# Kernel tuning notes

Hardware: AMD Instinct MI355X
Metric: run time of the kernel (lower is better)

## Reference

```python
import jax, jax.numpy as jnp
import numpy as np

B, E, K = 512, 4096, 1024      # batch, emb_dim, key_dim
M, L = 1024, 32                # mem_size, prompt_length
TOP_K = 4
EPS = 1e-12


def _l2norm(x, axis=-1):
    n = jnp.linalg.norm(x, axis=axis, keepdims=True)
    return x / jnp.maximum(n, EPS)


def setup_inputs() -> dict:
    key = jax.random.key(0)
    k1, k2, k3, k4 = jax.random.split(key, 4)
    return {
        "x_query": jax.random.normal(k1, (B, E), dtype=jnp.float32),
        "W_proj": jax.random.normal(k2, (K, E), dtype=jnp.float32) * 0.02,
        "prompt_memory": jax.random.normal(k3, (M, L, E), dtype=jnp.float32) * 0.02,
        "prompt_keys": jax.random.normal(k4, (M, K), dtype=jnp.float32) * 0.02,
        "top_k": TOP_K,
    }


def reference(x_query, W_proj, prompt_memory, prompt_keys, top_k):
    # x_proj = Linear(emb_dim -> key_dim, no bias): x @ W.T
    x_proj = jnp.einsum("be,ke->bk", x_query, W_proj)          # [B, K]
    x_norm = _l2norm(x_proj)                                     # [B, K]
    key_norm = _l2norm(prompt_keys)                              # [M, K]
    sim = jnp.einsum("bk,mk->bm", x_norm, key_norm)             # [B, M]
    _, idx = jax.lax.top_k(sim, top_k)                           # [B, top_k]
    sel_prompts = prompt_memory[idx]                             # [B, top_k, L, E]
    sel_keys = _l2norm(prompt_keys[idx], axis=2)                 # [B, top_k, K]
    refined = jnp.einsum("bk,btk->bt", x_norm, sel_keys)        # [B, top_k]
    w = jax.nn.softmax(refined, axis=1)                          # [B, top_k]
    # softmax-weighted sum over selected prompts
    out = jnp.einsum("btle,bt->ble", sel_prompts, w)            # [B, L, E]
    return out
```

## Files before the change

kernel.cpp:

```cpp
#include <hip/hip_runtime.h>
#include <math.h>

#define BDIM 512
#define EDIM 4096
#define KDIM 1024
#define MDIM 1024
#define LDIM 32
#define TOPK 4
#define EPSF 1e-12f

typedef __attribute__((ext_vector_type(8))) short short8;
typedef __attribute__((ext_vector_type(4))) float f32x4;

struct us4 { ushort x, y, z, w; };

__device__ inline ushort f2bf_rn(float x) {
    union { float f; unsigned u; } v; v.f = x;
    unsigned r = (v.u + 0x7FFF + ((v.u >> 16) & 1)) >> 16;
    return (ushort)r;
}
__device__ inline float bf2f(ushort h) {
    union { unsigned u; float f; } v; v.u = ((unsigned)h) << 16;
    return v.f;
}

__global__ __launch_bounds__(256)
void split_all_kernel(const float* __restrict__ xq, const float* __restrict__ wp,
                      const float* __restrict__ pk,
                      ushort* __restrict__ xq_h, ushort* __restrict__ xq_l,
                      ushort* __restrict__ wp_h, ushort* __restrict__ wp_l,
                      ushort* __restrict__ pk_h, ushort* __restrict__ pk_l,
                      float* __restrict__ kn)
{
    const int blk = blockIdx.x;
    const int t = threadIdx.x;
    const float* src; ushort* hi; ushort* lo; int base;
    bool do_norm = false; int rowbase = 0;
    if (blk < 512)       { src = xq; hi = xq_h; lo = xq_l; base = blk * 1024; }
    else if (blk < 1536) { src = wp; hi = wp_h; lo = wp_l; base = (blk - 512) * 1024; }
    else                 { src = pk; hi = pk_h; lo = pk_l; base = (blk - 1536) * 1024;
                           do_norm = true; rowbase = (blk - 1536) * 4; }

    __shared__ float wsum[4];
    const int lane = t & 63, wwid = t >> 6;

    #pragma unroll
    for (int it = 0; it < 4; ++it) {
        const int i = base + it * 256 + t;
        float4 v = ((const float4*)src)[i];
        us4 h, l;
        h.x = f2bf_rn(v.x); l.x = f2bf_rn(v.x - bf2f(h.x));
        h.y = f2bf_rn(v.y); l.y = f2bf_rn(v.y - bf2f(h.y));
        h.z = f2bf_rn(v.z); l.z = f2bf_rn(v.z - bf2f(h.z));
        h.w = f2bf_rn(v.w); l.w = f2bf_rn(v.w - bf2f(h.w));
        ((us4*)hi)[i] = h;
        ((us4*)lo)[i] = l;

        if (do_norm) {
            float sq = v.x * v.x + v.y * v.y + v.z * v.z + v.w * v.w;
            #pragma unroll
            for (int off = 32; off > 0; off >>= 1) sq += __shfl_down(sq, off, 64);
            __syncthreads();
            if (lane == 0) wsum[wwid] = sq;
            __syncthreads();
            if (t == 0)
                kn[rowbase + it] = sqrtf(wsum[0] + wsum[1] + wsum[2] + wsum[3]);
        }
    }
}

__global__ __launch_bounds__(256)
void gemm_mfma_split(const ushort* __restrict__ Ah, const ushort* __restrict__ Al,
                     const ushort* __restrict__ Bh, const ushort* __restrict__ Bl,
                     float* __restrict__ Cp, int M, int N, int K, int Kchunk)
{
    __shared__ ushort lds[4][64][40];

    const int t  = threadIdx.x;
    const int bn = blockIdx.x, bm = blockIdx.y, kz = blockIdx.z;

    const int srow = t >> 2, sg = t & 3;
    const size_t aoff = (size_t)(bm * 64 + srow) * K + sg * 8 + (size_t)kz * Kchunk;
    const size_t boff = (size_t)(bn * 64 + srow) * K + sg * 8 + (size_t)kz * Kchunk;

    const int lane = t & 63, wid = t >> 6;
    const int wr = wid >> 1, wc = wid & 1;
    const int fr = lane & 15, fg = lane >> 4;

    f32x4 acc[2][2];
    #pragma unroll
    for (int i = 0; i < 2; ++i)
        #pragma unroll
        for (int j = 0; j < 2; ++j)
            acc[i][j] = (f32x4){0.f, 0.f, 0.f, 0.f};

    short8 pA0 = *(const short8*)(Ah + aoff);
    short8 pA1 = *(const short8*)(Al + aoff);
    short8 pB0 = *(const short8*)(Bh + boff);
    short8 pB1 = *(const short8*)(Bl + boff);

    for (int k0 = 0; k0 < Kchunk; k0 += 32) {
        *(short8*)(&lds[0][srow][sg * 8]) = pA0;
        *(short8*)(&lds[1][srow][sg * 8]) = pA1;
        *(short8*)(&lds[2][srow][sg * 8]) = pB0;
        *(short8*)(&lds[3][srow][sg * 8]) = pB1;
        __syncthreads();

        if (k0 + 32 < Kchunk) {
            pA0 = *(const short8*)(Ah + aoff + k0 + 32);
            pA1 = *(const short8*)(Al + aoff + k0 + 32);
            pB0 = *(const short8*)(Bh + boff + k0 + 32);
            pB1 = *(const short8*)(Bl + boff + k0 + 32);
        }

        short8 ah[2], al[2], bh[2], bl[2];
        #pragma unroll
        for (int i = 0; i < 2; ++i) {
            ah[i] = *(const short8*)(&lds[0][wr * 32 + i * 16 + fr][fg * 8]);
            al[i] = *(const short8*)(&lds[1][wr * 32 + i * 16 + fr][fg * 8]);
            bh[i] = *(const short8*)(&lds[2][wc * 32 + i * 16 + fr][fg * 8]);
            bl[i] = *(const short8*)(&lds[3][wc * 32 + i * 16 + fr][fg * 8]);
        }
        #pragma unroll
        for (int i = 0; i < 2; ++i)
            #pragma unroll
            for (int j = 0; j < 2; ++j) {
                acc[i][j] = __builtin_amdgcn_mfma_f32_16x16x32_bf16(ah[i], bh[j], acc[i][j], 0, 0, 0);
                acc[i][j] = __builtin_amdgcn_mfma_f32_16x16x32_bf16(ah[i], bl[j], acc[i][j], 0, 0, 0);
                acc[i][j] = __builtin_amdgcn_mfma_f32_16x16x32_bf16(al[i], bh[j], acc[i][j], 0, 0, 0);
            }
        __syncthreads();
    }

    float* Cz = Cp + (size_t)kz * M * N;
    #pragma unroll
    for (int i = 0; i < 2; ++i)
        #pragma unroll
        for (int j = 0; j < 2; ++j)
            #pragma unroll
            for (int q = 0; q < 4; ++q) {
                int orow = bm * 64 + wr * 32 + i * 16 + (lane >> 4) * 4 + q;
                int ocol = bn * 64 + wc * 32 + j * 16 + (lane & 15);
                Cz[(size_t)orow * N + ocol] = acc[i][j][q];
            }
}

__global__ __launch_bounds__(256)
void reduce_split_norm_kernel(const float* __restrict__ Cp,
                              ushort* __restrict__ xh, ushort* __restrict__ xl,
                              float* __restrict__ xn)
{
    const int b = blockIdx.x;
    const int i = b * 256 + threadIdx.x;
    const int n4 = BDIM * KDIM / 4;

    float4 s = ((const float4*)Cp)[i];
    #pragma unroll
    for (int z = 1; z < 4; ++z) {
        float4 v = ((const float4*)Cp)[(size_t)z * n4 + i];
        s.x += v.x; s.y += v.y; s.z += v.z; s.w += v.w;
    }

    us4 h, l;
    h.x = f2bf_rn(s.x); l.x = f2bf_rn(s.x - bf2f(h.x));
    h.y = f2bf_rn(s.y); l.y = f2bf_rn(s.y - bf2f(h.y));
    h.z = f2bf_rn(s.z); l.z = f2bf_rn(s.z - bf2f(h.z));
    h.w = f2bf_rn(s.w); l.w = f2bf_rn(s.w - bf2f(h.w));
    ((us4*)xh)[i] = h;
    ((us4*)xl)[i] = l;

    float sq = s.x * s.x + s.y * s.y + s.z * s.z + s.w * s.w;
    #pragma unroll
    for (int off = 32; off > 0; off >>= 1) sq += __shfl_down(sq, off, 64);
    __shared__ float wsum[4];
    const int lane = threadIdx.x & 63, wwid = threadIdx.x >> 6;
    if (lane == 0) wsum[wwid] = sq;
    __syncthreads();
    if (threadIdx.x == 0)
        xn[b] = sqrtf(wsum[0] + wsum[1] + wsum[2] + wsum[3]);
}

__device__ inline bool tk_better(float x, int ix, float y, int iy) {
    return (x > y) || (x == y && ix < iy);
}
__device__ inline void tk_insert(float (&v)[4], int (&id)[4], float x, int m) {
    if (tk_better(x, m, v[3], id[3])) {
        v[3] = x; id[3] = m;
        if (tk_better(v[3], id[3], v[2], id[2])) {
            float tv = v[2]; int ti = id[2]; v[2] = v[3]; id[2] = id[3]; v[3] = tv; id[3] = ti;
            if (tk_better(v[2], id[2], v[1], id[1])) {
                tv = v[1]; ti = id[1]; v[1] = v[2]; id[1] = id[2]; v[2] = tv; id[2] = ti;
                if (tk_better(v[1], id[1], v[0], id[0])) {
                    tv = v[0]; ti = id[0]; v[0] = v[1]; id[0] = id[1]; v[1] = tv; id[1] = ti;
                }
            }
        }
    }
}
__global__ __launch_bounds__(64)
void topk_scale_kernel(const float* __restrict__ Cp2, const float* __restrict__ xn,
                       const float* __restrict__ kn,
                       int* __restrict__ topi, float* __restrict__ topv)
{
    const int b = blockIdx.x;
    const int lane = threadIdx.x;
    const float sb = 1.f / fmaxf(xn[b], EPSF);
    const float* r0 = Cp2 + (size_t)b * MDIM;
    const float* r1 = Cp2 + (size_t)BDIM * MDIM + (size_t)b * MDIM;

    float v[4] = {-INFINITY, -INFINITY, -INFINITY, -INFINITY};
    int id[4] = {-1, -1, -1, -1};
    for (int j = 0; j < MDIM / 64; ++j) {
        int m = j * 64 + lane;
        float s = (r0[m] + r1[m]) * sb / fmaxf(kn[m], EPSF);
        tk_insert(v, id, s, m);
    }
    for (int off = 32; off >= 1; off >>= 1) {
        float pv[4]; int pi[4];
        #pragma unroll
        for (int q = 0; q < 4; ++q) {
            pv[q] = __shfl_xor(v[q], off, 64);
            pi[q] = __shfl_xor(id[q], off, 64);
        }
        #pragma unroll
        for (int q = 0; q < 4; ++q) tk_insert(v, id, pv[q], pi[q]);
    }
    if (lane == 0) {
        #pragma unroll
        for (int q = 0; q < 4; ++q) { topv[b * 4 + q] = v[q]; topi[b * 4 + q] = id[q]; }
    }
}

__global__ __launch_bounds__(256)
void gather_out_kernel(const float* __restrict__ pm, const int* __restrict__ topi,
                       const float* __restrict__ topv, float* __restrict__ out)
{
    const int bl = blockIdx.x;
    const int b = bl & (BDIM - 1);
    const int l = bl >> 9;

    const int j0 = topi[b * 4 + 0], j1 = topi[b * 4 + 1], j2 = topi[b * 4 + 2], j3 = topi[b * 4 + 3];
    const float r0 = topv[b * 4 + 0], r1 = topv[b * 4 + 1], r2 = topv[b * 4 + 2], r3 = topv[b * 4 + 3];
    const float mx = fmaxf(fmaxf(r0, r1), fmaxf(r2, r3));
    const float e0 = expf(r0 - mx), e1 = expf(r1 - mx), e2 = expf(r2 - mx), e3 = expf(r3 - mx);
    const float inv = 1.f / (e0 + e1 + e2 + e3);
    const float w0 = e0 * inv, w1 = e1 * inv, w2 = e2 * inv, w3 = e3 * inv;

    const f32x4* p0 = (const f32x4*)(pm + ((size_t)j0 * LDIM + l) * EDIM);
    const f32x4* p1 = (const f32x4*)(pm + ((size_t)j1 * LDIM + l) * EDIM);
    const f32x4* p2 = (const f32x4*)(pm + ((size_t)j2 * LDIM + l) * EDIM);
    const f32x4* p3 = (const f32x4*)(pm + ((size_t)j3 * LDIM + l) * EDIM);
    f32x4* o = (f32x4*)(out + ((size_t)b * LDIM + l) * EDIM);

    for (int c = threadIdx.x; c < EDIM / 4; c += 256) {
        f32x4 a = p0[c], bb = p1[c], cc = p2[c], dd = p3[c];
        f32x4 r = w0 * a + w1 * bb + w2 * cc + w3 * dd;
        __builtin_nontemporal_store(r, &o[c]);
    }
}

extern "C" void kernel_launch(void* const* d_in, const int* in_sizes, int n_in,
                              void* d_out, int out_size, void* d_ws, size_t ws_size,
                              hipStream_t stream)
{
    const float* x_query = (const float*)d_in[0];
    const float* W_proj  = (const float*)d_in[1];
    const float* pm      = (const float*)d_in[2];
    const float* pkeys   = (const float*)d_in[3];
    float* out = (float*)d_out;

    char* w = (char*)d_ws;
    ushort* xq_h = (ushort*)w; w += (size_t)BDIM * EDIM * 2;
    ushort* xq_l = (ushort*)w; w += (size_t)BDIM * EDIM * 2;
    ushort* wp_h = (ushort*)w; w += (size_t)KDIM * EDIM * 2;
    ushort* wp_l = (ushort*)w; w += (size_t)KDIM * EDIM * 2;
    ushort* pk_h = (ushort*)w; w += (size_t)MDIM * KDIM * 2;
    ushort* pk_l = (ushort*)w; w += (size_t)MDIM * KDIM * 2;
    ushort* xp_h = (ushort*)w; w += (size_t)BDIM * KDIM * 2;
    ushort* xp_l = (ushort*)w; w += (size_t)BDIM * KDIM * 2;
    float* Cp1    = (float*)w; w += (size_t)4 * BDIM * KDIM * 4;
    float* Cp2    = (float*)w; w += (size_t)2 * BDIM * MDIM * 4;
    float* xn     = (float*)w; w += BDIM * 4;
    float* kn     = (float*)w; w += MDIM * 4;
    float* topv   = (float*)w; w += BDIM * TOPK * 4;
    int*   topi   = (int*)w;   w += BDIM * TOPK * 4;

    split_all_kernel<<<1792, 256, 0, stream>>>(
        x_query, W_proj, pkeys, xq_h, xq_l, wp_h, wp_l, pk_h, pk_l, kn);

    gemm_mfma_split<<<dim3(KDIM / 64, BDIM / 64, 4), 256, 0, stream>>>(
        xq_h, xq_l, wp_h, wp_l, Cp1, BDIM, KDIM, EDIM, EDIM / 4);

    reduce_split_norm_kernel<<<BDIM, 256, 0, stream>>>(Cp1, xp_h, xp_l, xn);

    gemm_mfma_split<<<dim3(MDIM / 64, BDIM / 64, 2), 256, 0, stream>>>(
        xp_h, xp_l, pk_h, pk_l, Cp2, BDIM, MDIM, KDIM, KDIM / 2);

    topk_scale_kernel<<<BDIM, 64, 0, stream>>>(Cp2, xn, kn, topi, topv);

    gather_out_kernel<<<BDIM * LDIM, 256, 0, stream>>>(pm, topi, topv, out);
}
```

Measured before the change: 240.3 us.

## Fuse bf16 hi/lo splitting into GEMM tile loads and drop split kernels

The separate split kernel and reduce-split kernel go away. Each GEMM now loads fp32 operands directly and splits them into bf16 hi/lo pairs while staging tiles into LDS. The second GEMM also sums the four split-K partials of the projection on the fly, and norm computation moves into a small combined kernel. The softmax weights are computed once per row in the top-k kernel instead of once per gather block. This removes kernel launches and the write and reread of the bf16 workspaces. In exchange the GEMM inner loops do more conversion arithmetic, read twice as many bytes per tile, and gemm2 reads four partial buffers redundantly across column blocks.

After: 248.4 us. +3.4%, slower.

```diff
diff --git a/kernel.cpp b/kernel.cpp
--- a/kernel.cpp
+++ b/kernel.cpp
@@ -12,8 +12,6 @@
 typedef __attribute__((ext_vector_type(8))) short short8;
 typedef __attribute__((ext_vector_type(4))) float f32x4;
 
-struct us4 { ushort x, y, z, w; };
-
 __device__ inline ushort f2bf_rn(float x) {
     union { float f; unsigned u; } v; v.f = x;
     unsigned r = (v.u + 0x7FFF + ((v.u >> 16) & 1)) >> 16;
@@ -23,65 +21,31 @@
     union { unsigned u; float f; } v; v.u = ((unsigned)h) << 16;
     return v.f;
 }
+__device__ inline void split8(const float4& v0, const float4& v1,
+                              short8& h, short8& l)
+{
+    float f[8] = {v0.x, v0.y, v0.z, v0.w, v1.x, v1.y, v1.z, v1.w};
+    #pragma unroll
+    for (int e = 0; e < 8; ++e) {
+        ushort hh = f2bf_rn(f[e]);
+        h[e] = (short)hh;
+        l[e] = (short)f2bf_rn(f[e] - bf2f(hh));
+    }
+}
 
 __global__ __launch_bounds__(256)
-void split_all_kernel(const float* __restrict__ xq, const float* __restrict__ wp,
-                      const float* __restrict__ pk,
-                      ushort* __restrict__ xq_h, ushort* __restrict__ xq_l,
-                      ushort* __restrict__ wp_h, ushort* __restrict__ wp_l,
-                      ushort* __restrict__ pk_h, ushort* __restrict__ pk_l,
-                      float* __restrict__ kn)
-{
-    const int blk = blockIdx.x;
-    const int t = threadIdx.x;
-    const float* src; ushort* hi; ushort* lo; int base;
-    bool do_norm = false; int rowbase = 0;
-    if (blk < 512)       { src = xq; hi = xq_h; lo = xq_l; base = blk * 1024; }
-    else if (blk < 1536) { src = wp; hi = wp_h; lo = wp_l; base = (blk - 512) * 1024; }
-    else                 { src = pk; hi = pk_h; lo = pk_l; base = (blk - 1536) * 1024;
-                           do_norm = true; rowbase = (blk - 1536) * 4; }
-
-    __shared__ float wsum[4];
-    const int lane = t & 63, wwid = t >> 6;
-
-    #pragma unroll
-    for (int it = 0; it < 4; ++it) {
-        const int i = base + it * 256 + t;
-        float4 v = ((const float4*)src)[i];
-        us4 h, l;
-        h.x = f2bf_rn(v.x); l.x = f2bf_rn(v.x - bf2f(h.x));
-        h.y = f2bf_rn(v.y); l.y = f2bf_rn(v.y - bf2f(h.y));
-        h.z = f2bf_rn(v.z); l.z = f2bf_rn(v.z - bf2f(h.z));
-        h.w = f2bf_rn(v.w); l.w = f2bf_rn(v.w - bf2f(h.w));
-        ((us4*)hi)[i] = h;
-        ((us4*)lo)[i] = l;
-
-        if (do_norm) {
-            float sq = v.x * v.x + v.y * v.y + v.z * v.z + v.w * v.w;
-            #pragma unroll
-            for (int off = 32; off > 0; off >>= 1) sq += __shfl_down(sq, off, 64);
-            __syncthreads();
-            if (lane == 0) wsum[wwid] = sq;
-            __syncthreads();
-            if (t == 0)
-                kn[rowbase + it] = sqrtf(wsum[0] + wsum[1] + wsum[2] + wsum[3]);
-        }
-    }
-}
-
-__global__ __launch_bounds__(256)
-void gemm_mfma_split(const ushort* __restrict__ Ah, const ushort* __restrict__ Al,
-                     const ushort* __restrict__ Bh, const ushort* __restrict__ Bl,
-                     float* __restrict__ Cp, int M, int N, int K, int Kchunk)
+void gemm1_kernel(const float* __restrict__ A, const float* __restrict__ B,
+                  float* __restrict__ Cp)
 {
     __shared__ ushort lds[4][64][40];
 
     const int t  = threadIdx.x;
     const int bn = blockIdx.x, bm = blockIdx.y, kz = blockIdx.z;
-
     const int srow = t >> 2, sg = t & 3;
-    const size_t aoff = (size_t)(bm * 64 + srow) * K + sg * 8 + (size_t)kz * Kchunk;
-    const size_t boff = (size_t)(bn * 64 + srow) * K + sg * 8 + (size_t)kz * Kchunk;
+    const int Kc = EDIM / 4;
+
+    const float* Ap = A + (size_t)(bm * 64 + srow) * EDIM + kz * Kc + sg * 8;
+    const float* Bp = B + (size_t)(bn * 64 + srow) * EDIM + kz * Kc + sg * 8;
 
     const int lane = t & 63, wid = t >> 6;
     const int wr = wid >> 1, wc = wid & 1;
@@ -94,23 +58,22 @@
         for (int j = 0; j < 2; ++j)
             acc[i][j] = (f32x4){0.f, 0.f, 0.f, 0.f};
 
-    short8 pA0 = *(const short8*)(Ah + aoff);
-    short8 pA1 = *(const short8*)(Al + aoff);
-    short8 pB0 = *(const short8*)(Bh + boff);
-    short8 pB1 = *(const short8*)(Bl + boff);
-
-    for (int k0 = 0; k0 < Kchunk; k0 += 32) {
-        *(short8*)(&lds[0][srow][sg * 8]) = pA0;
-        *(short8*)(&lds[1][srow][sg * 8]) = pA1;
-        *(short8*)(&lds[2][srow][sg * 8]) = pB0;
-        *(short8*)(&lds[3][srow][sg * 8]) = pB1;
+    float4 a0 = *(const float4*)(Ap),     a1 = *(const float4*)(Ap + 4);
+    float4 b0 = *(const float4*)(Bp),     b1 = *(const float4*)(Bp + 4);
+
+    for (int k0 = 0; k0 < Kc; k0 += 32) {
+        short8 ahs, als, bhs, bls;
+        split8(a0, a1, ahs, als);
+        split8(b0, b1, bhs, bls);
+        *(short8*)(&lds[0][srow][sg * 8]) = ahs;
+        *(short8*)(&lds[1][srow][sg * 8]) = als;
+        *(short8*)(&lds[2][srow][sg * 8]) = bhs;
+        *(short8*)(&lds[3][srow][sg * 8]) = bls;
         __syncthreads();
 
-        if (k0 + 32 < Kchunk) {
-            pA0 = *(const short8*)(Ah + aoff + k0 + 32);
-            pA1 = *(const short8*)(Al + aoff + k0 + 32);
-            pB0 = *(const short8*)(Bh + boff + k0 + 32);
-            pB1 = *(const short8*)(Bl + boff + k0 + 32);
+        if (k0 + 32 < Kc) {
+            a0 = *(const float4*)(Ap + k0 + 32); a1 = *(const float4*)(Ap + k0 + 36);
+            b0 = *(const float4*)(Bp + k0 + 32); b1 = *(const float4*)(Bp + k0 + 36);
         }
 
         short8 ah[2], al[2], bh[2], bl[2];
@@ -132,7 +95,7 @@
         __syncthreads();
     }
 
-    float* Cz = Cp + (size_t)kz * M * N;
+    float* Cz = Cp + (size_t)kz * BDIM * KDIM;
     #pragma unroll
     for (int i = 0; i < 2; ++i)
         #pragma unroll
@@ -141,43 +104,134 @@
             for (int q = 0; q < 4; ++q) {
                 int orow = bm * 64 + wr * 32 + i * 16 + (lane >> 4) * 4 + q;
                 int ocol = bn * 64 + wc * 32 + j * 16 + (lane & 15);
-                Cz[(size_t)orow * N + ocol] = acc[i][j][q];
+                Cz[(size_t)orow * KDIM + ocol] = acc[i][j][q];
             }
 }
 
 __global__ __launch_bounds__(256)
-void reduce_split_norm_kernel(const float* __restrict__ Cp,
-                              ushort* __restrict__ xh, ushort* __restrict__ xl,
-                              float* __restrict__ xn)
-{
-    const int b = blockIdx.x;
-    const int i = b * 256 + threadIdx.x;
-    const int n4 = BDIM * KDIM / 4;
-
-    float4 s = ((const float4*)Cp)[i];
-    #pragma unroll
-    for (int z = 1; z < 4; ++z) {
-        float4 v = ((const float4*)Cp)[(size_t)z * n4 + i];
-        s.x += v.x; s.y += v.y; s.z += v.z; s.w += v.w;
-    }
-
-    us4 h, l;
-    h.x = f2bf_rn(s.x); l.x = f2bf_rn(s.x - bf2f(h.x));
-    h.y = f2bf_rn(s.y); l.y = f2bf_rn(s.y - bf2f(h.y));
-    h.z = f2bf_rn(s.z); l.z = f2bf_rn(s.z - bf2f(h.z));
-    h.w = f2bf_rn(s.w); l.w = f2bf_rn(s.w - bf2f(h.w));
-    ((us4*)xh)[i] = h;
-    ((us4*)xl)[i] = l;
-
-    float sq = s.x * s.x + s.y * s.y + s.z * s.z + s.w * s.w;
+void gemm2_kernel(const float* __restrict__ Cp1, const float* __restrict__ PK,
+                  float* __restrict__ Cp2)
+{
+    __shared__ ushort lds[4][64][40];
+
+    const int t  = threadIdx.x;
+    const int bn = blockIdx.x, bm = blockIdx.y, kz = blockIdx.z;
+    const int srow = t >> 2, sg = t & 3;
+    const int Kc = KDIM / 2;
+    const size_t ZS = (size_t)BDIM * KDIM;
+
+    const float* Ap = Cp1 + (size_t)(bm * 64 + srow) * KDIM + kz * Kc + sg * 8;
+    const float* Bp = PK  + (size_t)(bn * 64 + srow) * KDIM + kz * Kc + sg * 8;
+
+    const int lane = t & 63, wid = t >> 6;
+    const int wr = wid >> 1, wc = wid & 1;
+    const int fr = lane & 15, fg = lane >> 4;
+
+    f32x4 acc[2][2];
+    #pragma unroll
+    for (int i = 0; i < 2; ++i)
+        #pragma unroll
+        for (int j = 0; j < 2; ++j)
+            acc[i][j] = (f32x4){0.f, 0.f, 0.f, 0.f};
+
+    float4 pa0[4], pa1[4], pb0, pb1;
+    #pragma unroll
+    for (int z = 0; z < 4; ++z) {
+        pa0[z] = *(const float4*)(Ap + z * ZS);
+        pa1[z] = *(const float4*)(Ap + z * ZS + 4);
+    }
+    pb0 = *(const float4*)(Bp);
+    pb1 = *(const float4*)(Bp + 4);
+
+    for (int k0 = 0; k0 < Kc; k0 += 32) {
+        float4 s0 = pa0[0], s1 = pa1[0];
+        #pragma unroll
+        for (int z = 1; z < 4; ++z) {
+            s0.x += pa0[z].x; s0.y += pa0[z].y; s0.z += pa0[z].z; s0.w += pa0[z].w;
+            s1.x += pa1[z].x; s1.y += pa1[z].y; s1.z += pa1[z].z; s1.w += pa1[z].w;
+        }
+        short8 ahs, als, bhs, bls;
+        split8(s0, s1, ahs, als);
+        split8(pb0, pb1, bhs, bls);
+        *(short8*)(&lds[0][srow][sg * 8]) = ahs;
+        *(short8*)(&lds[1][srow][sg * 8]) = als;
+        *(short8*)(&lds[2][srow][sg * 8]) = bhs;
+        *(short8*)(&lds[3][srow][sg * 8]) = bls;
+        __syncthreads();
+
+        if (k0 + 32 < Kc) {
+            #pragma unroll
+            for (int z = 0; z < 4; ++z) {
+                pa0[z] = *(const float4*)(Ap + z * ZS + k0 + 32);
+                pa1[z] = *(const float4*)(Ap + z * ZS + k0 + 36);
+            }
+            pb0 = *(const float4*)(Bp + k0 + 32);
+            pb1 = *(const float4*)(Bp + k0 + 36);
+        }
+
+        short8 ah[2], al[2], bh[2], bl[2];
+        #pragma unroll
+        for (int i = 0; i < 2; ++i) {
+            ah[i] = *(const short8*)(&lds[0][wr * 32 + i * 16 + fr][fg * 8]);
+            al[i] = *(const short8*)(&lds[1][wr * 32 + i * 16 + fr][fg * 8]);
+            bh[i] = *(const short8*)(&lds[2][wc * 32 + i * 16 + fr][fg * 8]);
+            bl[i] = *(const short8*)(&lds[3][wc * 32 + i * 16 + fr][fg * 8]);
+        }
+        #pragma unroll
+        for (int i = 0; i < 2; ++i)
+            #pragma unroll
+            for (int j = 0; j < 2; ++j) {
+                acc[i][j] = __builtin_amdgcn_mfma_f32_16x16x32_bf16(ah[i], bh[j], acc[i][j], 0, 0, 0);
+                acc[i][j] = __builtin_amdgcn_mfma_f32_16x16x32_bf16(ah[i], bl[j], acc[i][j], 0, 0, 0);
+                acc[i][j] = __builtin_amdgcn_mfma_f32_16x16x32_bf16(al[i], bh[j], acc[i][j], 0, 0, 0);
+            }
+        __syncthreads();
+    }
+
+    float* Cz = Cp2 + (size_t)kz * BDIM * MDIM;
+    #pragma unroll
+    for (int i = 0; i < 2; ++i)
+        #pragma unroll
+        for (int j = 0; j < 2; ++j)
+            #pragma unroll
+            for (int q = 0; q < 4; ++q) {
+                int orow = bm * 64 + wr * 32 + i * 16 + (lane >> 4) * 4 + q;
+                int ocol = bn * 64 + wc * 32 + j * 16 + (lane & 15);
+                Cz[(size_t)orow * MDIM + ocol] = acc[i][j][q];
+            }
+}
+
+__global__ __launch_bounds__(256)
+void norms_kernel(const float* __restrict__ PK, const float* __restrict__ Cp1,
+                  float* __restrict__ kn, float* __restrict__ xn)
+{
+    const int blk = blockIdx.x, t = threadIdx.x;
+    float sq;
+    if (blk < MDIM) {
+        float4 v = *(const float4*)(PK + (size_t)blk * KDIM + t * 4);
+        sq = v.x * v.x + v.y * v.y + v.z * v.z + v.w * v.w;
+    } else {
+        const int b = blk - MDIM;
+        const int i = b * 256 + t;
+        const int n4 = BDIM * KDIM / 4;
+        float4 s = ((const float4*)Cp1)[i];
+        #pragma unroll
+        for (int z = 1; z < 4; ++z) {
+            float4 v = ((const float4*)Cp1)[(size_t)z * n4 + i];
+            s.x += v.x; s.y += v.y; s.z += v.z; s.w += v.w;
+        }
+        sq = s.x * s.x + s.y * s.y + s.z * s.z + s.w * s.w;
+    }
     #pragma unroll
     for (int off = 32; off > 0; off >>= 1) sq += __shfl_down(sq, off, 64);
     __shared__ float wsum[4];
-    const int lane = threadIdx.x & 63, wwid = threadIdx.x >> 6;
+    const int lane = t & 63, wwid = t >> 6;
     if (lane == 0) wsum[wwid] = sq;
     __syncthreads();
-    if (threadIdx.x == 0)
-        xn[b] = sqrtf(wsum[0] + wsum[1] + wsum[2] + wsum[3]);
+    if (t == 0) {
+        float r = sqrtf(wsum[0] + wsum[1] + wsum[2] + wsum[3]);
+        if (blk < MDIM) kn[blk] = r; else xn[blk - MDIM] = r;
+    }
 }
 
 __device__ inline bool tk_better(float x, int ix, float y, int iy) {
@@ -200,7 +254,7 @@
 __global__ __launch_bounds__(64)
 void topk_scale_kernel(const float* __restrict__ Cp2, const float* __restrict__ xn,
                        const float* __restrict__ kn,
-                       int* __restrict__ topi, float* __restrict__ topv)
+                       int* __restrict__ topi, float* __restrict__ topw)
 {
     const int b = blockIdx.x;
     const int lane = threadIdx.x;
@@ -226,25 +280,27 @@
         for (int q = 0; q < 4; ++q) tk_insert(v, id, pv[q], pi[q]);
     }
     if (lane == 0) {
-        #pragma unroll
-        for (int q = 0; q < 4; ++q) { topv[b * 4 + q] = v[q]; topi[b * 4 + q] = id[q]; }
+        const float mx = fmaxf(fmaxf(v[0], v[1]), fmaxf(v[2], v[3]));
+        const float e0 = expf(v[0] - mx), e1 = expf(v[1] - mx);
+        const float e2 = expf(v[2] - mx), e3 = expf(v[3] - mx);
+        const float inv = 1.f / (e0 + e1 + e2 + e3);
+        topw[b * 4 + 0] = e0 * inv; topw[b * 4 + 1] = e1 * inv;
+        topw[b * 4 + 2] = e2 * inv; topw[b * 4 + 3] = e3 * inv;
+        #pragma unroll
+        for (int q = 0; q < 4; ++q) topi[b * 4 + q] = id[q];
     }
 }
 
 __global__ __launch_bounds__(256)
 void gather_out_kernel(const float* __restrict__ pm, const int* __restrict__ topi,
-                       const float* __restrict__ topv, float* __restrict__ out)
+                       const float* __restrict__ topw, float* __restrict__ out)
 {
     const int bl = blockIdx.x;
     const int b = bl & (BDIM - 1);
     const int l = bl >> 9;
 
     const int j0 = topi[b * 4 + 0], j1 = topi[b * 4 + 1], j2 = topi[b * 4 + 2], j3 = topi[b * 4 + 3];
-    const float r0 = topv[b * 4 + 0], r1 = topv[b * 4 + 1], r2 = topv[b * 4 + 2], r3 = topv[b * 4 + 3];
-    const float mx = fmaxf(fmaxf(r0, r1), fmaxf(r2, r3));
-    const float e0 = expf(r0 - mx), e1 = expf(r1 - mx), e2 = expf(r2 - mx), e3 = expf(r3 - mx);
-    const float inv = 1.f / (e0 + e1 + e2 + e3);
-    const float w0 = e0 * inv, w1 = e1 * inv, w2 = e2 * inv, w3 = e3 * inv;
+    const float w0 = topw[b * 4 + 0], w1 = topw[b * 4 + 1], w2 = topw[b * 4 + 2], w3 = topw[b * 4 + 3];
 
     const f32x4* p0 = (const f32x4*)(pm + ((size_t)j0 * LDIM + l) * EDIM);
     const f32x4* p1 = (const f32x4*)(pm + ((size_t)j1 * LDIM + l) * EDIM);
@@ -270,33 +326,22 @@
     float* out = (float*)d_out;
 
     char* w = (char*)d_ws;
-    ushort* xq_h = (ushort*)w; w += (size_t)BDIM * EDIM * 2;
-    ushort* xq_l = (ushort*)w; w += (size_t)BDIM * EDIM * 2;
-    ushort* wp_h = (ushort*)w; w += (size_t)KDIM * EDIM * 2;
-    ushort* wp_l = (ushort*)w; w += (size_t)KDIM * EDIM * 2;
-    ushort* pk_h = (ushort*)w; w += (size_t)MDIM * KDIM * 2;
-    ushort* pk_l = (ushort*)w; w += (size_t)MDIM * KDIM * 2;
-    ushort* xp_h = (ushort*)w; w += (size_t)BDIM * KDIM * 2;
-    ushort* xp_l = (ushort*)w; w += (size_t)BDIM * KDIM * 2;
-    float* Cp1    = (float*)w; w += (size_t)4 * BDIM * KDIM * 4;
-    float* Cp2    = (float*)w; w += (size_t)2 * BDIM * MDIM * 4;
-    float* xn     = (float*)w; w += BDIM * 4;
-    float* kn     = (float*)w; w += MDIM * 4;
-    float* topv   = (float*)w; w += BDIM * TOPK * 4;
-    int*   topi   = (int*)w;   w += BDIM * TOPK * 4;
-
-    split_all_kernel<<<1792, 256, 0, stream>>>(
-        x_query, W_proj, pkeys, xq_h, xq_l, wp_h, wp_l, pk_h, pk_l, kn);
-
-    gemm_mfma_split<<<dim3(KDIM / 64, BDIM / 64, 4), 256, 0, stream>>>(
-        xq_h, xq_l, wp_h, wp_l, Cp1, BDIM, KDIM, EDIM, EDIM / 4);
-
-    reduce_split_norm_kernel<<<BDIM, 256, 0, stream>>>(Cp1, xp_h, xp_l, xn);
-
-    gemm_mfma_split<<<dim3(MDIM / 64, BDIM / 64, 2), 256, 0, stream>>>(
-        xp_h, xp_l, pk_h, pk_l, Cp2, BDIM, MDIM, KDIM, KDIM / 2);
-
-    topk_scale_kernel<<<BDIM, 64, 0, stream>>>(Cp2, xn, kn, topi, topv);
-
-    gather_out_kernel<<<BDIM * LDIM, 256, 0, stream>>>(pm, topi, topv, out);
-}
+    float* Cp1  = (float*)w; w += (size_t)4 * BDIM * KDIM * 4;
+    float* Cp2  = (float*)w; w += (size_t)2 * BDIM * MDIM * 4;
+    float* xn   = (float*)w; w += BDIM * 4;
+    float* kn   = (float*)w; w += MDIM * 4;
+    float* topw = (float*)w; w += BDIM * TOPK * 4;
+    int*   topi = (int*)w;   w += BDIM * TOPK * 4;
+
+    gemm1_kernel<<<dim3(KDIM / 64, BDIM / 64, 4), 256, 0, stream>>>(
+        x_query, W_proj, Cp1);
+
+    norms_kernel<<<MDIM + BDIM, 256, 0, stream>>>(pkeys, Cp1, kn, xn);
+
+    gemm2_kernel<<<dim3(MDIM / 64, BDIM / 64, 2), 256, 0, stream>>>(
+        Cp1, pkeys, Cp2);
+
+    topk_scale_kernel<<<BDIM, 64, 0, stream>>>(Cp2, xn, kn, topi, topw);
+
+    gather_out_kernel<<<BDIM * LDIM, 256, 0, stream>>>(pm, topi, topw, out);
+}
```
